# Kernel optimization log

Measured on AMD Instinct MI355X. Metric: run time of the kernel, lower is better.

## Reference

```python
import jax, jax.numpy as jnp
import numpy as np

B, L, D, H = 2, 384, 256, 8
DH = D // H


def setup_inputs() -> dict:
    key = jax.random.key(0)
    ks = jax.random.split(key, 16)
    xav = lambda k, shape: jax.random.normal(k, shape, jnp.float32) * np.sqrt(2.0 / sum(shape[-2:]))
    return {
        "key": jax.random.normal(ks[0], (B, L, D), jnp.float32),
        "query": jax.random.normal(ks[1], (B, L, D), jnp.float32),
        "value": jax.random.normal(ks[2], (B, L, D), jnp.float32),
        "pos": jax.random.normal(ks[3], (B, L, L, D), jnp.float32),
        "key_mask": jnp.ones((B, L), jnp.float32),
        "Wk": xav(ks[4], (D, D)), "bk": jnp.zeros((D,), jnp.float32),
        "Wq": xav(ks[5], (D, D)), "bq": jnp.zeros((D,), jnp.float32),
        "Wv": xav(ks[6], (D, D)), "bv": jnp.zeros((D,), jnp.float32),
        "Wr": xav(ks[7], (D, D)), "br": jnp.zeros((D,), jnp.float32),
        "u": xav(ks[8], (H, DH)),
        "v": xav(ks[9], (H, DH)),
    }


def reference(key, query, value, pos, key_mask, Wk, bk, Wq, bq, Wv, bv, Wr, br, u, v):
    b, l, d = key.shape
    dh = d // H
    # projections (torch Linear: x @ W.T + b)
    k = (key @ Wk.T + bk).reshape(b, l, H, dh).transpose(0, 2, 1, 3)    # [b,h,l,dh]
    q = (query @ Wq.T + bq).reshape(b, l, H, dh).transpose(0, 2, 1, 3)  # [b,h,l,dh]
    val = (value @ Wv.T + bv).reshape(b, l, H, dh).transpose(0, 2, 1, 3)
    r = (pos @ Wr.T + br).reshape(b, l, l, H, dh)                       # [b,q,k,h,dh]
    # content term A+C: (q + u) @ k^T
    A_C = jnp.einsum("bhqd,bhkd->bhqk", q + u[None, :, None, :], k)
    # position term B+D: (q + v) contracted with per-(q,k) relative embedding
    B_D = jnp.einsum("bhqd,bqkhd->bhqk", q + v[None, :, None, :], r)
    score = (A_C + B_D) / np.sqrt(dh).astype(np.float32)
    score = score - (1.0 - key_mask[:, None, None, :]) * 1e15
    attn = jax.nn.softmax(score, axis=-1)  # dropout is identity at eval
    out = jnp.einsum("bhqk,bhkd->bhqd", attn, val)
    return out.transpose(0, 2, 1, 3).reshape(b, l, d)
```

## Files before the change

kernel.cpp:

```cpp
#include <hip/hip_runtime.h>
#include <math.h>

#define BB 2
#define LL 384
#define DD 256
#define HH 8
#define DHH 32

static const size_t OFF_Q     = 0;
static const size_t OFF_KK    = 196608;
static const size_t OFF_VV    = 393216;
static const size_t OFF_W     = 589824;
static const size_t OFF_CBR   = 2162688;
static const size_t OFF_SCORE = 2168832;

__device__ __forceinline__ float dot4(float4 a, float4 b) {
    return a.x * b.x + a.y * b.y + a.z * b.z + a.w * b.w;
}

__global__ __launch_bounds__(256) void k_proj(
    const float* __restrict__ Xq, const float* __restrict__ Xk, const float* __restrict__ Xv,
    const float* __restrict__ Wq, const float* __restrict__ Wk, const float* __restrict__ Wv,
    const float* __restrict__ bq, const float* __restrict__ bk, const float* __restrict__ bv,
    float* __restrict__ oq, float* __restrict__ okk, float* __restrict__ ovv)
{
    int bx = blockIdx.x;
    int mat = bx / 96;
    int rem = bx % 96;
    int b = rem / 48;
    int l0 = (rem % 48) * 8;
    const float* X = (mat == 0) ? Xq : (mat == 1) ? Xk : Xv;
    const float* W = (mat == 0) ? Wq : (mat == 1) ? Wk : Wv;
    const float* bias = (mat == 0) ? bq : (mat == 1) ? bk : bv;

    __shared__ float xs[8 * 256];
    int tid = threadIdx.x;
    {
        const float4* src = (const float4*)(X + (size_t)(b * LL + l0) * DD);
        float4* dst = (float4*)xs;
        dst[tid] = src[tid];
        dst[tid + 256] = src[tid + 256];
    }
    __syncthreads();

    int n = tid;
    float bn = bias[n];
    float acc[8];
#pragma unroll
    for (int l = 0; l < 8; ++l) acc[l] = bn;

    const float4* wrow = (const float4*)(W + (size_t)n * DD);
#pragma unroll 8
    for (int kc = 0; kc < 64; ++kc) {
        float4 wv = wrow[kc];
#pragma unroll
        for (int l = 0; l < 8; ++l) {
            float4 xv = ((const float4*)(xs + l * 256))[kc];
            acc[l] += dot4(wv, xv);
        }
    }

    if (mat <= 1) {
        float* o = (mat == 0) ? oq : okk;
#pragma unroll
        for (int l = 0; l < 8; ++l)
            o[(size_t)(b * LL + l0 + l) * DD + n] = acc[l];
    } else {
        int h = n >> 5, dh = n & 31;
#pragma unroll
        for (int l = 0; l < 8; ++l)
            ovv[((size_t)(b * HH + h) * LL + l0 + l) * DHH + dh] = acc[l];
    }
}

__global__ __launch_bounds__(256) void k_wproj(
    const float* __restrict__ q, const float* __restrict__ vpar,
    const float* __restrict__ Wr, const float* __restrict__ br,
    float* __restrict__ w, float* __restrict__ cbr)
{
    int bx = blockIdx.x;
    int b = bx / 384;
    int rem = bx % 384;
    int l0 = (rem >> 2) * 4;
    int hg = rem & 3;
    int tid = threadIdx.x;
    int gq = tid >> 6;
    int lane = tid & 63;

    __shared__ float qv[4][64];
    if (lane < 16) {
        const float* qsrc = q + (size_t)(b * LL + l0 + gq) * DD + hg * 64;
        const float* vsrc = vpar + hg * 64;
        float4 t = *(const float4*)(qsrc + lane * 4);
        float4 vv4 = *(const float4*)(vsrc + lane * 4);
        t.x += vv4.x; t.y += vv4.y; t.z += vv4.z; t.w += vv4.w;
        *(float4*)(&qv[gq][lane * 4]) = t;
    }
    __syncthreads();

    int l = l0 + gq;
    int d4 = lane * 4;
    float* wbase = w + ((size_t)(b * LL + l) * HH) * DD + d4;
#pragma unroll
    for (int h2 = 0; h2 < 2; ++h2) {
        int h = hg * 2 + h2;
        float4 acc = make_float4(0.f, 0.f, 0.f, 0.f);
#pragma unroll 8
        for (int dh = 0; dh < 32; ++dh) {
            float s = qv[gq][h2 * 32 + dh];
            float4 wr4 = *(const float4*)(Wr + (size_t)(h * 32 + dh) * DD + d4);
            acc.x += s * wr4.x; acc.y += s * wr4.y; acc.z += s * wr4.z; acc.w += s * wr4.w;
        }
        *(float4*)(wbase + h * DD) = acc;
    }

    if (tid < 8) {
        int rr = tid >> 1, h2 = tid & 1;
        float s = 0.f;
#pragma unroll 8
        for (int dh = 0; dh < 32; ++dh)
            s += qv[rr][h2 * 32 + dh] * br[hg * 64 + h2 * 32 + dh];
        cbr[(size_t)(b * LL + l0 + rr) * HH + hg * 2 + h2] = s;
    }
}

__global__ __launch_bounds__(256, 2) void k_bd(
    const float* __restrict__ pos, const float* __restrict__ w,
    const float* __restrict__ q, const float* __restrict__ u,
    const float* __restrict__ kk, const float* __restrict__ cbr,
    const float* __restrict__ mask, float* __restrict__ score)
{
    int b = blockIdx.x / LL;
    int qi = blockIdx.x % LL;
    int tid = threadIdx.x;
    int wave = tid >> 6;
    int lane = tid & 63;
    int g = lane & 15;
    int r = lane >> 4;

    const float* wb = w + ((size_t)(b * LL + qi) * HH) * DD + g * 4;
    float4 wr[8][4];
#pragma unroll
    for (int h = 0; h < 8; ++h) {
#pragma unroll
        for (int j = 0; j < 4; ++j)
            wr[h][j] = *(const float4*)(wb + h * DD + j * 64);
    }

    float2 qu[8];
    const float* qrow = q + (size_t)(b * LL + qi) * DD + 2 * g;
#pragma unroll
    for (int h = 0; h < 8; ++h) {
        float2 qa = *(const float2*)(qrow + h * 32);
        float2 ua = *(const float2*)(u + h * 32 + 2 * g);
        qu[h] = make_float2(qa.x + ua.x, qa.y + ua.y);
    }
    float cb[8];
#pragma unroll
    for (int h = 0; h < 8; ++h) cb[h] = cbr[(size_t)(b * LL + qi) * HH + h];

    const float* posq = pos + (size_t)(b * LL + qi) * LL * DD + g * 4;
    const float* kkb = kk + (size_t)b * LL * DD + 2 * g;
    float* sb = score + ((size_t)(b * HH) * LL + qi) * LL;
    const float inv = 0.17677669529663687f;

#pragma unroll 1
    for (int k0 = wave * 4; k0 < LL; k0 += 16) {
        int krow = k0 + r;
        const float* pr = posq + (size_t)krow * DD;
        float4 p0 = *(const float4*)(pr);
        float4 p1 = *(const float4*)(pr + 64);
        float4 p2 = *(const float4*)(pr + 128);
        float4 p3 = *(const float4*)(pr + 192);
        const float* kr = kkb + (size_t)krow * DD;
        float acc[8];
#pragma unroll
        for (int h = 0; h < 8; ++h) {
            float2 kv = *(const float2*)(kr + h * 32);
            acc[h] = dot4(p0, wr[h][0]) + dot4(p1, wr[h][1]) +
                     dot4(p2, wr[h][2]) + dot4(p3, wr[h][3]) +
                     qu[h].x * kv.x + qu[h].y * kv.y;
        }
#pragma unroll
        for (int m = 1; m <= 8; m <<= 1) {
#pragma unroll
            for (int h = 0; h < 8; ++h)
                acc[h] += __shfl_xor(acc[h], m, 64);
        }
        if (g == 0) {
            float pen = (1.0f - mask[b * LL + krow]) * 1e15f;
#pragma unroll
            for (int h = 0; h < 8; ++h)
                sb[(size_t)h * LL * LL + krow] = (acc[h] + cb[h]) * inv - pen;
        }
    }
}

__global__ __launch_bounds__(256) void k_softpv(
    const float* __restrict__ score, const float* __restrict__ vv,
    float* __restrict__ out)
{
    int bx = blockIdx.x;
    int qt = bx % 48;
    int bh = bx / 48;
    int b = bh >> 3;
    int h = bh & 7;
    int q0 = qt * 8;
    int tid = threadIdx.x;

    __shared__ float valT[32][388];
    __shared__ float attn[8][388];

    const float* vb = vv + (size_t)(b * HH + h) * LL * DHH;
    for (int i = 0; i < 48; ++i) {
        int flat = i * 256 + tid;
        valT[flat & 31][flat >> 5] = vb[flat];
    }

    int wave = tid >> 6, lane = tid & 63;
    for (int ri = 0; ri < 2; ++ri) {
        int ql = wave * 2 + ri;
        const float* srow = score + ((size_t)(b * HH + h) * LL + q0 + ql) * LL;
        float s[6];
#pragma unroll
        for (int j = 0; j < 6; ++j) s[j] = srow[lane + 64 * j];
        float m = s[0];
#pragma unroll
        for (int j = 1; j < 6; ++j) m = fmaxf(m, s[j]);
#pragma unroll
        for (int off = 1; off < 64; off <<= 1) m = fmaxf(m, __shfl_xor(m, off, 64));
        float e[6];
        float ls = 0.f;
#pragma unroll
        for (int j = 0; j < 6; ++j) { e[j] = __expf(s[j] - m); ls += e[j]; }
#pragma unroll
        for (int off = 1; off < 64; off <<= 1) ls += __shfl_xor(ls, off, 64);
        float rinv = 1.0f / ls;
#pragma unroll
        for (int j = 0; j < 6; ++j) attn[ql][lane + 64 * j] = e[j] * rinv;
    }
    __syncthreads();

    int dh = tid & 31, qp = tid >> 5;
    const float4* vrow = (const float4*)valT[dh];
    const float4* arow = (const float4*)attn[qp];
    float acc = 0.f;
    for (int k4 = 0; k4 < 96; ++k4) {
        acc += dot4(arow[k4], vrow[k4]);
    }
    out[(size_t)(b * LL + q0 + qp) * DD + h * 32 + dh] = acc;
}

extern "C" void kernel_launch(void* const* d_in, const int* in_sizes, int n_in,
                              void* d_out, int out_size, void* d_ws, size_t ws_size,
                              hipStream_t stream) {
    const float* key    = (const float*)d_in[0];
    const float* query  = (const float*)d_in[1];
    const float* value  = (const float*)d_in[2];
    const float* pos    = (const float*)d_in[3];
    const float* kmask  = (const float*)d_in[4];
    const float* Wk     = (const float*)d_in[5];
    const float* bk     = (const float*)d_in[6];
    const float* Wq     = (const float*)d_in[7];
    const float* bq     = (const float*)d_in[8];
    const float* Wv     = (const float*)d_in[9];
    const float* bv     = (const float*)d_in[10];
    const float* Wr     = (const float*)d_in[11];
    const float* br     = (const float*)d_in[12];
    const float* u      = (const float*)d_in[13];
    const float* v      = (const float*)d_in[14];
    float* out = (float*)d_out;

    float* ws = (float*)d_ws;
    float* qbuf   = ws + OFF_Q;
    float* kkbuf  = ws + OFF_KK;
    float* vvbuf  = ws + OFF_VV;
    float* wbuf   = ws + OFF_W;
    float* cbrbuf = ws + OFF_CBR;
    float* sbuf   = ws + OFF_SCORE;

    k_proj<<<dim3(288), dim3(256), 0, stream>>>(query, key, value, Wq, Wk, Wv,
                                                bq, bk, bv, qbuf, kkbuf, vvbuf);
    k_wproj<<<dim3(768), dim3(256), 0, stream>>>(qbuf, v, Wr, br, wbuf, cbrbuf);
    k_bd<<<dim3(768), dim3(256), 0, stream>>>(pos, wbuf, qbuf, u, kkbuf, cbrbuf,
                                              kmask, sbuf);
    k_softpv<<<dim3(768), dim3(256), 0, stream>>>(sbuf, vvbuf, out);
}
```

Baseline: 506.4 us.

## Fuse softmax and attention-value product into score kernel via shared memory

Merges the score computation with softmax and the P·V product so scores stay in shared memory instead of a global buffer, removing one kernel launch and the global score round trip. Each block now handles one query for all heads and reads V directly from global (L2) per key, which increases V traffic because it is no longer shared across multiple queries per block.

Result: no change. 502.9 us (-0.7%).

```diff
diff --git a/kernel.cpp b/kernel.cpp
--- a/kernel.cpp
+++ b/kernel.cpp
@@ -12,7 +12,6 @@
 static const size_t OFF_VV    = 393216;
 static const size_t OFF_W     = 589824;
 static const size_t OFF_CBR   = 2162688;
-static const size_t OFF_SCORE = 2168832;
 
 __device__ __forceinline__ float dot4(float4 a, float4 b) {
     return a.x * b.x + a.y * b.y + a.z * b.z + a.w * b.w;
@@ -124,11 +123,12 @@
     }
 }
 
-__global__ __launch_bounds__(256, 2) void k_bd(
+__global__ __launch_bounds__(256, 2) void k_bdsoft(
     const float* __restrict__ pos, const float* __restrict__ w,
     const float* __restrict__ q, const float* __restrict__ u,
     const float* __restrict__ kk, const float* __restrict__ cbr,
-    const float* __restrict__ mask, float* __restrict__ score)
+    const float* __restrict__ mask, const float* __restrict__ vv,
+    float* __restrict__ out)
 {
     int b = blockIdx.x / LL;
     int qi = blockIdx.x % LL;
@@ -138,6 +138,8 @@
     int g = lane & 15;
     int r = lane >> 4;
 
+    __shared__ float sld[8][388];
+
     const float* wb = w + ((size_t)(b * LL + qi) * HH) * DD + g * 4;
     float4 wr[8][4];
 #pragma unroll
@@ -161,7 +163,6 @@
 
     const float* posq = pos + (size_t)(b * LL + qi) * LL * DD + g * 4;
     const float* kkb = kk + (size_t)b * LL * DD + 2 * g;
-    float* sb = score + ((size_t)(b * HH) * LL + qi) * LL;
     const float inv = 0.17677669529663687f;
 
 #pragma unroll 1
@@ -191,39 +192,17 @@
             float pen = (1.0f - mask[b * LL + krow]) * 1e15f;
 #pragma unroll
             for (int h = 0; h < 8; ++h)
-                sb[(size_t)h * LL * LL + krow] = (acc[h] + cb[h]) * inv - pen;
-        }
-    }
-}
-
-__global__ __launch_bounds__(256) void k_softpv(
-    const float* __restrict__ score, const float* __restrict__ vv,
-    float* __restrict__ out)
-{
-    int bx = blockIdx.x;
-    int qt = bx % 48;
-    int bh = bx / 48;
-    int b = bh >> 3;
-    int h = bh & 7;
-    int q0 = qt * 8;
-    int tid = threadIdx.x;
-
-    __shared__ float valT[32][388];
-    __shared__ float attn[8][388];
-
-    const float* vb = vv + (size_t)(b * HH + h) * LL * DHH;
-    for (int i = 0; i < 48; ++i) {
-        int flat = i * 256 + tid;
-        valT[flat & 31][flat >> 5] = vb[flat];
-    }
-
-    int wave = tid >> 6, lane = tid & 63;
-    for (int ri = 0; ri < 2; ++ri) {
-        int ql = wave * 2 + ri;
-        const float* srow = score + ((size_t)(b * HH + h) * LL + q0 + ql) * LL;
+                sld[h][krow] = (acc[h] + cb[h]) * inv - pen;
+        }
+    }
+    __syncthreads();
+
+#pragma unroll
+    for (int hi = 0; hi < 2; ++hi) {
+        int h = wave * 2 + hi;
         float s[6];
 #pragma unroll
-        for (int j = 0; j < 6; ++j) s[j] = srow[lane + 64 * j];
+        for (int j = 0; j < 6; ++j) s[j] = sld[h][lane + 64 * j];
         float m = s[0];
 #pragma unroll
         for (int j = 1; j < 6; ++j) m = fmaxf(m, s[j]);
@@ -237,18 +216,18 @@
         for (int off = 1; off < 64; off <<= 1) ls += __shfl_xor(ls, off, 64);
         float rinv = 1.0f / ls;
 #pragma unroll
-        for (int j = 0; j < 6; ++j) attn[ql][lane + 64 * j] = e[j] * rinv;
-    }
-    __syncthreads();
-
-    int dh = tid & 31, qp = tid >> 5;
-    const float4* vrow = (const float4*)valT[dh];
-    const float4* arow = (const float4*)attn[qp];
+        for (int j = 0; j < 6; ++j) sld[h][lane + 64 * j] = e[j] * rinv;
+    }
+    __syncthreads();
+
+    int h = tid >> 5, dh = tid & 31;
+    const float* vp = vv + ((size_t)(b * HH + h) * LL) * DHH + dh;
     float acc = 0.f;
-    for (int k4 = 0; k4 < 96; ++k4) {
-        acc += dot4(arow[k4], vrow[k4]);
-    }
-    out[(size_t)(b * LL + q0 + qp) * DD + h * 32 + dh] = acc;
+#pragma unroll 8
+    for (int k = 0; k < LL; ++k) {
+        acc += sld[h][k] * vp[(size_t)k * DHH];
+    }
+    out[(size_t)(b * LL + qi) * DD + tid] = acc;
 }
 
 extern "C" void kernel_launch(void* const* d_in, const int* in_sizes, int n_in,
@@ -277,12 +256,10 @@
     float* vvbuf  = ws + OFF_VV;
     float* wbuf   = ws + OFF_W;
     float* cbrbuf = ws + OFF_CBR;
-    float* sbuf   = ws + OFF_SCORE;
 
     k_proj<<<dim3(288), dim3(256), 0, stream>>>(query, key, value, Wq, Wk, Wv,
                                                 bq, bk, bv, qbuf, kkbuf, vvbuf);
     k_wproj<<<dim3(768), dim3(256), 0, stream>>>(qbuf, v, Wr, br, wbuf, cbrbuf);
-    k_bd<<<dim3(768), dim3(256), 0, stream>>>(pos, wbuf, qbuf, u, kkbuf, cbrbuf,
-                                              kmask, sbuf);
-    k_softpv<<<dim3(768), dim3(256), 0, stream>>>(sbuf, vvbuf, out);
-}
+    k_bdsoft<<<dim3(768), dim3(256), 0, stream>>>(pos, wbuf, qbuf, u, kkbuf,
+                                                  cbrbuf, kmask, vvbuf, out);
+}
```
